# Kernel tuning notes

Measured on AMD Instinct MI355X. Metric: run time of the kernel, lower is better.

Reference implementation:

```python
import jax, jax.numpy as jnp
import numpy as np

B, S = 16, 32768
LEVELS = (5, 20)
TIME_DIM = 8
NUM_FREQS = 6  # frequency xyz encoder: 3*(1+2*6)=39 dims
HID = 128
IN_DIM = 3 * (1 + 2 * NUM_FREQS) + 2 * TIME_DIM  # 55


def setup_inputs() -> dict:
    key = jax.random.key(0)
    ks = jax.random.split(key, 16)
    time = jax.random.uniform(ks[0], (B,), dtype=jnp.float32)
    xyz = jax.random.uniform(ks[1], (B, S, 3), dtype=jnp.float32) * 2.0 - 1.0  # in [-1,1]
    te0 = jax.random.normal(ks[2], (LEVELS[0] + 1, TIME_DIM), dtype=jnp.float32)
    te1 = jax.random.normal(ks[3], (LEVELS[1] + 1, TIME_DIM), dtype=jnp.float32)
    W0 = jax.random.normal(ks[4], (IN_DIM, HID), dtype=jnp.float32) * 0.05
    b0 = jnp.zeros((HID,), dtype=jnp.float32)
    W1 = jax.random.normal(ks[5], (HID, HID), dtype=jnp.float32) * 0.05
    b1 = jnp.zeros((HID,), dtype=jnp.float32)
    W2 = jax.random.normal(ks[6], (HID, HID), dtype=jnp.float32) * 0.05
    b2 = jnp.zeros((HID,), dtype=jnp.float32)
    Wout = jax.random.normal(ks[7], (HID, 1), dtype=jnp.float32) * 0.05
    bout = jnp.zeros((1,), dtype=jnp.float32)
    return {"time": time, "xyz": xyz, "te0": te0, "te1": te1,
            "W0": W0, "b0": b0, "W1": W1, "b1": b1, "W2": W2, "b2": b2,
            "Wout": Wout, "bout": bout}


def _time_encode(t, emb, L):
    # bucketize t into L uniform intervals on [0,1), lerp between bucket endpoints
    tL = t * L
    idx = jnp.clip(jnp.floor(tL).astype(jnp.int32), 0, L - 1)  # (B,)
    w = (idx + 1).astype(t.dtype) - tL                          # weight for lower endpoint
    lerped = w[:, None] * emb[idx] + (1.0 - w)[:, None] * emb[idx + 1]
    # t >= 1: use last embedding directly (torch fallback branch)
    return jnp.where((t >= 1.0)[:, None], emb[L][None, :], lerped)


def _xyz_encode(x):
    # frequency encoding, include_input, freqs 2^0..2^(NUM_FREQS-1)
    freqs = jnp.asarray(2.0 ** np.arange(NUM_FREQS), dtype=x.dtype)  # (F,)
    xp = x[:, None, :] * freqs[None, :, None]                         # (N, F, 3)
    n = x.shape[0]
    return jnp.concatenate([x, jnp.sin(xp).reshape(n, -1), jnp.cos(xp).reshape(n, -1)], axis=-1)


def reference(time, xyz, te0, te1, W0, b0, W1, b1, W2, b2, Wout, bout):
    s = xyz.shape[1]
    t_enc = jnp.concatenate([_time_encode(time, te0, LEVELS[0]),
                             _time_encode(time, te1, LEVELS[1])], axis=-1)  # (B, 16)
    t_enc = jnp.repeat(t_enc, s, axis=0)          # (B*S, 16)  'B d -> (B S) d'
    pts = (xyz.reshape(-1, 3) + 1.0) / 2.0        # (B*S, 3)
    x = jnp.concatenate([t_enc, _xyz_encode(pts)], axis=1)  # (B*S, 55)
    x = jax.nn.relu(x @ W0 + b0)
    x = jax.nn.relu(x @ W1 + b1)
    x = jax.nn.relu(x @ W2 + b2)
    return x @ Wout + bout  # (B*S, 1)
```

## Files before the change

### kernel.cpp

```cpp
#include <hip/hip_runtime.h>

typedef _Float16 f16;
typedef __attribute__((ext_vector_type(2))) __fp16 fp16x2;
typedef __attribute__((ext_vector_type(8))) _Float16 f16x8;
typedef __attribute__((ext_vector_type(4))) float f32x4;
typedef __attribute__((ext_vector_type(4))) unsigned int u32x4;

#define NPTS   (16 * 32768)
#define W0P_OFF 0
#define W1P_OFF (16 * 1024)
#define W2P_OFF (48 * 1024)
#define WOP_OFF (80 * 1024)
#define FRAGS_BYTES (84 * 1024)
#define B0E_OFF FRAGS_BYTES
#define WS_NEEDED (FRAGS_BYTES + 8192)
#define LDS_TOTAL 4096

__global__ void pack_weights(const float* __restrict__ time, const float* __restrict__ te0,
                             const float* __restrict__ te1, const float* __restrict__ W0,
                             const float* __restrict__ b0, const float* __restrict__ W1,
                             const float* __restrict__ W2, const float* __restrict__ Wout,
                             unsigned char* __restrict__ ws) {
  const int bi = blockIdx.x;
  const int l = threadIdx.x;
  const int g = l >> 4, r16 = l & 15;
  if (bi < 84) {
    const float* W; int obase, fi, kt, mt, kmax; bool natural, outcol;
    if (bi < 16)      { W = W0;   fi = bi;      mt = fi >> 1; kt = fi & 1; obase = W0P_OFF; kmax = 39;  natural = true;  outcol = false; }
    else if (bi < 48) { W = W1;   fi = bi - 16; mt = fi >> 2; kt = fi & 3; obase = W1P_OFF; kmax = 128; natural = false; outcol = false; }
    else if (bi < 80) { W = W2;   fi = bi - 48; mt = fi >> 2; kt = fi & 3; obase = W2P_OFF; kmax = 128; natural = false; outcol = false; }
    else              { W = Wout; fi = bi - 80; mt = 0;       kt = fi;     obase = WOP_OFF; kmax = 128; natural = false; outcol = true;  }
    const int m = mt * 16 + r16;
    f16 vals[8] __attribute__((aligned(16)));
#pragma unroll
    for (int j = 0; j < 8; ++j) {
      const int k = natural ? (kt * 32 + g * 8 + j)
                            : (kt * 32 + (j >> 2) * 16 + g * 4 + (j & 3));
      float v = 0.f;
      if (k < kmax) {
        if (outcol)       v = (m == 0) ? Wout[k] : 0.f;
        else if (natural) v = W[(16 + k) * 128 + m];
        else              v = W[k * 128 + m];
      }
      vals[j] = (f16)v;
    }
    *(u32x4*)(ws + obase + (fi * 64 + l) * 16) = *(const u32x4*)vals;
  } else {
    const int idx = (bi - 84) * 64 + l;
    const int b = idx >> 7, m = idx & 127;
    const float t = time[b];
    float acc = b0[m];
#pragma unroll
    for (int d = 0; d < 16; ++d) {
      const float* emb; int L, dd;
      if (d < 8) { emb = te0; L = 5;  dd = d; }
      else       { emb = te1; L = 20; dd = d - 8; }
      const float tL = t * (float)L;
      int i = (int)floorf(tL);
      i = i < 0 ? 0 : (i > L - 1 ? L - 1 : i);
      const float wlo = (float)(i + 1) - tL;
      float v = wlo * emb[i * 8 + dd] + (1.f - wlo) * emb[(i + 1) * 8 + dd];
      if (t >= 1.f) v = emb[L * 8 + dd];
      acc += v * W0[d * 128 + m];
    }
    ((float*)(ws + B0E_OFF))[b * 128 + m] = acc;
  }
}

__device__ __forceinline__ unsigned int pkmax0(unsigned int x) {
  unsigned int r;
  asm("v_pk_max_f16 %0, %1, %2" : "=v"(r) : "v"(x), "v"(0u));
  return r;
}
__device__ __forceinline__ unsigned int pkrtz(float a, float b) {
  union { fp16x2 h; unsigned int u; } c;
  c.h = __builtin_amdgcn_cvt_pkrtz(a, b);
  return c.u;
}
__device__ __forceinline__ float hwsin_rev(float rev) {
  float r; asm("v_sin_f32 %0, %1" : "=v"(r) : "v"(rev)); return r;
}
__device__ __forceinline__ float hwcos_rev(float rev) {
  float r; asm("v_cos_f32 %0, %1" : "=v"(r) : "v"(rev)); return r;
}

template <int KT>
__device__ __forceinline__ void layer_swapped(const unsigned char* __restrict__ wsrc,
                                              const float* __restrict__ bias,
                                              const f16x8 (&Bin)[KT][4], f16x8 (&Bout)[4][4],
                                              int lane) {
  const int g4 = (lane >> 4) * 4;
  f16x8 A0b[3], A1b[3];
  float4 ba, bb;
  f32x4 acc[2][4];
#pragma unroll
  for (int s = 0; s < 2; ++s) {
    const int mtp = s / KT, kt = s % KT;
    A0b[s] = *(const f16x8*)(wsrc + (((2 * mtp)     * KT + kt) * 64 + lane) * 16);
    A1b[s] = *(const f16x8*)(wsrc + (((2 * mtp + 1) * KT + kt) * 64 + lane) * 16);
  }
#pragma unroll
  for (int s = 0; s < 4 * KT; ++s) {
    const int mtp = s / KT, kt = s % KT, cb = s % 3;
    if (kt == 0) {
      ba = *(const float4*)(bias + mtp * 32 + g4);
      bb = *(const float4*)(bias + mtp * 32 + 16 + g4);
#pragma unroll
      for (int nt = 0; nt < 4; ++nt) {
        acc[0][nt] = (f32x4){ba.x, ba.y, ba.z, ba.w};
        acc[1][nt] = (f32x4){bb.x, bb.y, bb.z, bb.w};
      }
    }
    if (s + 2 < 4 * KT) {
      const int mtp2 = (s + 2) / KT, kt2 = (s + 2) % KT, pb = (s + 2) % 3;
      A0b[pb] = *(const f16x8*)(wsrc + (((2 * mtp2)     * KT + kt2) * 64 + lane) * 16);
      A1b[pb] = *(const f16x8*)(wsrc + (((2 * mtp2 + 1) * KT + kt2) * 64 + lane) * 16);
    }
    __builtin_amdgcn_s_setprio(1);
#pragma unroll
    for (int nt = 0; nt < 4; ++nt)
      acc[0][nt] = __builtin_amdgcn_mfma_f32_16x16x32_f16(A0b[cb], Bin[kt][nt], acc[0][nt], 0, 0, 0);
#pragma unroll
    for (int nt = 0; nt < 4; ++nt)
      acc[1][nt] = __builtin_amdgcn_mfma_f32_16x16x32_f16(A1b[cb], Bin[kt][nt], acc[1][nt], 0, 0, 0);
    __builtin_amdgcn_s_setprio(0);
    if (kt == KT - 1) {
#pragma unroll
      for (int nt = 0; nt < 4; ++nt) {
        union { unsigned int w[4]; f16x8 v; } u;
        u.w[0] = pkmax0(pkrtz(acc[0][nt][0], acc[0][nt][1]));
        u.w[1] = pkmax0(pkrtz(acc[0][nt][2], acc[0][nt][3]));
        u.w[2] = pkmax0(pkrtz(acc[1][nt][0], acc[1][nt][1]));
        u.w[3] = pkmax0(pkrtz(acc[1][nt][2], acc[1][nt][3]));
        Bout[mtp][nt] = u.v;
      }
    }
  }
}

__global__ void __launch_bounds__(64, 1)
mlp_main(const float* __restrict__ xyz, const float* __restrict__ b1,
         const float* __restrict__ b2, const float* __restrict__ bout,
         const unsigned char* __restrict__ ws, float* __restrict__ out) {
  extern __shared__ char lds[];
  const int lane = threadIdx.x;
  const int g = lane >> 4, r16 = lane & 15;

  char* scr = lds;
  const float bo = bout[0];

  const int pbase = blockIdx.x * 64;
  const int p = pbase + lane;

  float ff[40];
  const float xs0 = xyz[p * 3], xs1 = xyz[p * 3 + 1], xs2 = xyz[p * 3 + 2];
  const float pcs[3] = {(xs0 + 1.f) * 0.5f, (xs1 + 1.f) * 0.5f, (xs2 + 1.f) * 0.5f};
  const float INV2PI = 0.15915494309189535f;
#pragma unroll
  for (int c = 0; c < 3; ++c) {
    ff[c] = pcs[c];
    const float rev = pcs[c] * INV2PI;
    float s = hwsin_rev(rev), co = hwcos_rev(rev);
#pragma unroll
    for (int f = 0; f < 6; ++f) {
      ff[3 + f * 3 + c] = s;
      ff[21 + f * 3 + c] = co;
      const float s2 = 2.f * s * co, c2 = 1.f - 2.f * s * s;
      s = s2; co = c2;
    }
  }
  ff[39] = 0.f;
  unsigned int fw[32];
#pragma unroll
  for (int i = 0; i < 20; ++i) fw[i] = pkrtz(ff[2 * i], ff[2 * i + 1]);
#pragma unroll
  for (int i = 20; i < 32; ++i) fw[i] = 0u;

  f16x8 B0[2][4];
#pragma unroll
  for (int h = 0; h < 2; ++h) {
    if ((lane >> 5) == h) {
#pragma unroll
      for (int s = 0; s < 8; ++s)
        *(u32x4*)(scr + (lane & 31) * 128 + ((s ^ (lane & 7)) * 16)) = ((const u32x4*)fw)[s];
    }
    asm volatile("s_waitcnt lgkmcnt(0)" ::: "memory");
#pragma unroll
    for (int kt = 0; kt < 2; ++kt)
#pragma unroll
      for (int nn = 0; nn < 2; ++nn) {
        const int row = nn * 16 + r16;
        B0[kt][h * 2 + nn] = *(const f16x8*)(scr + row * 128 + (((4 * kt + g) ^ (row & 7)) * 16));
      }
    asm volatile("s_waitcnt lgkmcnt(0)" ::: "memory");
  }

  const float* b0e = (const float*)(ws + B0E_OFF) + (blockIdx.x >> 9) * 128;
  f16x8 Bx[4][4], By[4][4];
  layer_swapped<2>(ws + W0P_OFF, b0e, B0, Bx, lane);
  layer_swapped<4>(ws + W1P_OFF, b1, Bx, By, lane);
  layer_swapped<4>(ws + W2P_OFF, b2, By, Bx, lane);

  f16x8 Ab[4];
#pragma unroll
  for (int kt = 0; kt < 4; ++kt)
    Ab[kt] = *(const f16x8*)(ws + WOP_OFF + (kt * 64 + lane) * 16);
  const f32x4 bovec = (f32x4){bo, bo, bo, bo};
  f32x4 accO[4];
  __builtin_amdgcn_s_setprio(1);
#pragma unroll
  for (int nt = 0; nt < 4; ++nt)
    accO[nt] = __builtin_amdgcn_mfma_f32_16x16x32_f16(Ab[0], Bx[0][nt], bovec, 0, 0, 0);
#pragma unroll
  for (int kt = 1; kt < 4; ++kt) {
#pragma unroll
    for (int nt = 0; nt < 4; ++nt)
      accO[nt] = __builtin_amdgcn_mfma_f32_16x16x32_f16(Ab[kt], Bx[kt][nt], accO[nt], 0, 0, 0);
  }
  __builtin_amdgcn_s_setprio(0);

  const float a0 = __shfl(accO[0][0], r16, 64);
  const float a1 = __shfl(accO[1][0], r16, 64);
  const float a2 = __shfl(accO[2][0], r16, 64);
  const float a3 = __shfl(accO[3][0], r16, 64);
  const float v = g == 0 ? a0 : g == 1 ? a1 : g == 2 ? a2 : a3;
  out[pbase + lane] = v;
}

extern "C" void kernel_launch(void* const* d_in, const int* in_sizes, int n_in,
                              void* d_out, int out_size, void* d_ws, size_t ws_size,
                              hipStream_t stream) {
  const float* time = (const float*)d_in[0];
  const float* xyz  = (const float*)d_in[1];
  const float* te0  = (const float*)d_in[2];
  const float* te1  = (const float*)d_in[3];
  const float* W0   = (const float*)d_in[4];
  const float* b0   = (const float*)d_in[5];
  const float* W1   = (const float*)d_in[6];
  const float* b1   = (const float*)d_in[7];
  const float* W2   = (const float*)d_in[8];
  const float* b2   = (const float*)d_in[9];
  const float* Wout = (const float*)d_in[10];
  const float* bout = (const float*)d_in[11];
  float* out = (float*)d_out;
  unsigned char* ws = (unsigned char*)d_ws;
  if (ws_size < WS_NEEDED) return;

  pack_weights<<<116, 64, 0, stream>>>(time, te0, te1, W0, b0, W1, W2, Wout, ws);
  mlp_main<<<NPTS / 64, 64, LDS_TOTAL, stream>>>(xyz, b1, b2, bout, ws, out);
}
```

Measured before the change: 46.87 us.

## Process two 64-point tiles per wave to reuse weight fragments across MFMAs

Each single-wave block now handles 128 points as two 64-point tiles. Every loaded weight fragment feeds MFMAs for both tiles, halving weight traffic per point and giving the MFMA pipe more independent work per load. The number of blocks halves, and the time-embedding bias index is adjusted to match. The cost is roughly double the accumulator and activation register footprint, which could cause spills or lower occupancy.

```diff
diff --git a/kernel.cpp b/kernel.cpp
--- a/kernel.cpp
+++ b/kernel.cpp
@@ -85,14 +85,15 @@
 }
 
 template <int KT>
-__device__ __forceinline__ void layer_swapped(const unsigned char* __restrict__ wsrc,
-                                              const float* __restrict__ bias,
-                                              const f16x8 (&Bin)[KT][4], f16x8 (&Bout)[4][4],
-                                              int lane) {
+__device__ __forceinline__ void layer_dual(const unsigned char* __restrict__ wsrc,
+                                           const float* __restrict__ bias,
+                                           const f16x8 (&Bin0)[KT][4], const f16x8 (&Bin1)[KT][4],
+                                           f16x8 (&Bout0)[4][4], f16x8 (&Bout1)[4][4],
+                                           int lane) {
   const int g4 = (lane >> 4) * 4;
   f16x8 A0b[3], A1b[3];
   float4 ba, bb;
-  f32x4 acc[2][4];
+  f32x4 acc0[2][4], acc1[2][4];
 #pragma unroll
   for (int s = 0; s < 2; ++s) {
     const int mtp = s / KT, kt = s % KT;
@@ -107,8 +108,10 @@
       bb = *(const float4*)(bias + mtp * 32 + 16 + g4);
 #pragma unroll
       for (int nt = 0; nt < 4; ++nt) {
-        acc[0][nt] = (f32x4){ba.x, ba.y, ba.z, ba.w};
-        acc[1][nt] = (f32x4){bb.x, bb.y, bb.z, bb.w};
+        acc0[0][nt] = (f32x4){ba.x, ba.y, ba.z, ba.w};
+        acc0[1][nt] = (f32x4){bb.x, bb.y, bb.z, bb.w};
+        acc1[0][nt] = (f32x4){ba.x, ba.y, ba.z, ba.w};
+        acc1[1][nt] = (f32x4){bb.x, bb.y, bb.z, bb.w};
       }
     }
     if (s + 2 < 4 * KT) {
@@ -119,20 +122,31 @@
     __builtin_amdgcn_s_setprio(1);
 #pragma unroll
     for (int nt = 0; nt < 4; ++nt)
-      acc[0][nt] = __builtin_amdgcn_mfma_f32_16x16x32_f16(A0b[cb], Bin[kt][nt], acc[0][nt], 0, 0, 0);
-#pragma unroll
-    for (int nt = 0; nt < 4; ++nt)
-      acc[1][nt] = __builtin_amdgcn_mfma_f32_16x16x32_f16(A1b[cb], Bin[kt][nt], acc[1][nt], 0, 0, 0);
+      acc0[0][nt] = __builtin_amdgcn_mfma_f32_16x16x32_f16(A0b[cb], Bin0[kt][nt], acc0[0][nt], 0, 0, 0);
+#pragma unroll
+    for (int nt = 0; nt < 4; ++nt)
+      acc1[0][nt] = __builtin_amdgcn_mfma_f32_16x16x32_f16(A0b[cb], Bin1[kt][nt], acc1[0][nt], 0, 0, 0);
+#pragma unroll
+    for (int nt = 0; nt < 4; ++nt)
+      acc0[1][nt] = __builtin_amdgcn_mfma_f32_16x16x32_f16(A1b[cb], Bin0[kt][nt], acc0[1][nt], 0, 0, 0);
+#pragma unroll
+    for (int nt = 0; nt < 4; ++nt)
+      acc1[1][nt] = __builtin_amdgcn_mfma_f32_16x16x32_f16(A1b[cb], Bin1[kt][nt], acc1[1][nt], 0, 0, 0);
     __builtin_amdgcn_s_setprio(0);
     if (kt == KT - 1) {
 #pragma unroll
       for (int nt = 0; nt < 4; ++nt) {
-        union { unsigned int w[4]; f16x8 v; } u;
-        u.w[0] = pkmax0(pkrtz(acc[0][nt][0], acc[0][nt][1]));
-        u.w[1] = pkmax0(pkrtz(acc[0][nt][2], acc[0][nt][3]));
-        u.w[2] = pkmax0(pkrtz(acc[1][nt][0], acc[1][nt][1]));
-        u.w[3] = pkmax0(pkrtz(acc[1][nt][2], acc[1][nt][3]));
-        Bout[mtp][nt] = u.v;
+        union { unsigned int w[4]; f16x8 v; } u0, u1;
+        u0.w[0] = pkmax0(pkrtz(acc0[0][nt][0], acc0[0][nt][1]));
+        u0.w[1] = pkmax0(pkrtz(acc0[0][nt][2], acc0[0][nt][3]));
+        u0.w[2] = pkmax0(pkrtz(acc0[1][nt][0], acc0[1][nt][1]));
+        u0.w[3] = pkmax0(pkrtz(acc0[1][nt][2], acc0[1][nt][3]));
+        u1.w[0] = pkmax0(pkrtz(acc1[0][nt][0], acc1[0][nt][1]));
+        u1.w[1] = pkmax0(pkrtz(acc1[0][nt][2], acc1[0][nt][3]));
+        u1.w[2] = pkmax0(pkrtz(acc1[1][nt][0], acc1[1][nt][1]));
+        u1.w[3] = pkmax0(pkrtz(acc1[1][nt][2], acc1[1][nt][3]));
+        Bout0[mtp][nt] = u0.v;
+        Bout1[mtp][nt] = u1.v;
       }
     }
   }
@@ -149,82 +163,97 @@
   char* scr = lds;
   const float bo = bout[0];
 
-  const int pbase = blockIdx.x * 64;
-  const int p = pbase + lane;
-
-  float ff[40];
-  const float xs0 = xyz[p * 3], xs1 = xyz[p * 3 + 1], xs2 = xyz[p * 3 + 2];
-  const float pcs[3] = {(xs0 + 1.f) * 0.5f, (xs1 + 1.f) * 0.5f, (xs2 + 1.f) * 0.5f};
+  const int pbase = blockIdx.x * 128;
+
+  f16x8 B0[2][2][4];
   const float INV2PI = 0.15915494309189535f;
 #pragma unroll
-  for (int c = 0; c < 3; ++c) {
-    ff[c] = pcs[c];
-    const float rev = pcs[c] * INV2PI;
-    float s = hwsin_rev(rev), co = hwcos_rev(rev);
-#pragma unroll
-    for (int f = 0; f < 6; ++f) {
-      ff[3 + f * 3 + c] = s;
-      ff[21 + f * 3 + c] = co;
-      const float s2 = 2.f * s * co, c2 = 1.f - 2.f * s * s;
-      s = s2; co = c2;
-    }
-  }
-  ff[39] = 0.f;
-  unsigned int fw[32];
-#pragma unroll
-  for (int i = 0; i < 20; ++i) fw[i] = pkrtz(ff[2 * i], ff[2 * i + 1]);
-#pragma unroll
-  for (int i = 20; i < 32; ++i) fw[i] = 0u;
-
-  f16x8 B0[2][4];
-#pragma unroll
-  for (int h = 0; h < 2; ++h) {
-    if ((lane >> 5) == h) {
-#pragma unroll
-      for (int s = 0; s < 8; ++s)
-        *(u32x4*)(scr + (lane & 31) * 128 + ((s ^ (lane & 7)) * 16)) = ((const u32x4*)fw)[s];
-    }
-    asm volatile("s_waitcnt lgkmcnt(0)" ::: "memory");
-#pragma unroll
-    for (int kt = 0; kt < 2; ++kt)
-#pragma unroll
-      for (int nn = 0; nn < 2; ++nn) {
-        const int row = nn * 16 + r16;
-        B0[kt][h * 2 + nn] = *(const f16x8*)(scr + row * 128 + (((4 * kt + g) ^ (row & 7)) * 16));
-      }
-    asm volatile("s_waitcnt lgkmcnt(0)" ::: "memory");
-  }
-
-  const float* b0e = (const float*)(ws + B0E_OFF) + (blockIdx.x >> 9) * 128;
-  f16x8 Bx[4][4], By[4][4];
-  layer_swapped<2>(ws + W0P_OFF, b0e, B0, Bx, lane);
-  layer_swapped<4>(ws + W1P_OFF, b1, Bx, By, lane);
-  layer_swapped<4>(ws + W2P_OFF, b2, By, Bx, lane);
+  for (int t = 0; t < 2; ++t) {
+    const int p = pbase + t * 64 + lane;
+    float ff[40];
+    const float xs0 = xyz[p * 3], xs1 = xyz[p * 3 + 1], xs2 = xyz[p * 3 + 2];
+    const float pcs[3] = {(xs0 + 1.f) * 0.5f, (xs1 + 1.f) * 0.5f, (xs2 + 1.f) * 0.5f};
+#pragma unroll
+    for (int c = 0; c < 3; ++c) {
+      ff[c] = pcs[c];
+      const float rev = pcs[c] * INV2PI;
+      float s = hwsin_rev(rev), co = hwcos_rev(rev);
+#pragma unroll
+      for (int f = 0; f < 6; ++f) {
+        ff[3 + f * 3 + c] = s;
+        ff[21 + f * 3 + c] = co;
+        const float s2 = 2.f * s * co, c2 = 1.f - 2.f * s * s;
+        s = s2; co = c2;
+      }
+    }
+    ff[39] = 0.f;
+    unsigned int fw[32];
+#pragma unroll
+    for (int i = 0; i < 20; ++i) fw[i] = pkrtz(ff[2 * i], ff[2 * i + 1]);
+#pragma unroll
+    for (int i = 20; i < 32; ++i) fw[i] = 0u;
+
+#pragma unroll
+    for (int h = 0; h < 2; ++h) {
+      if ((lane >> 5) == h) {
+#pragma unroll
+        for (int s = 0; s < 8; ++s)
+          *(u32x4*)(scr + (lane & 31) * 128 + ((s ^ (lane & 7)) * 16)) = ((const u32x4*)fw)[s];
+      }
+      asm volatile("s_waitcnt lgkmcnt(0)" ::: "memory");
+#pragma unroll
+      for (int kt = 0; kt < 2; ++kt)
+#pragma unroll
+        for (int nn = 0; nn < 2; ++nn) {
+          const int row = nn * 16 + r16;
+          B0[t][kt][h * 2 + nn] = *(const f16x8*)(scr + row * 128 + (((4 * kt + g) ^ (row & 7)) * 16));
+        }
+      asm volatile("s_waitcnt lgkmcnt(0)" ::: "memory");
+    }
+  }
+
+  const float* b0e = (const float*)(ws + B0E_OFF) + (blockIdx.x >> 8) * 128;
+  f16x8 Bx0[4][4], Bx1[4][4], By0[4][4], By1[4][4];
+  layer_dual<2>(ws + W0P_OFF, b0e, B0[0], B0[1], Bx0, Bx1, lane);
+  layer_dual<4>(ws + W1P_OFF, b1, Bx0, Bx1, By0, By1, lane);
+  layer_dual<4>(ws + W2P_OFF, b2, By0, By1, Bx0, Bx1, lane);
 
   f16x8 Ab[4];
 #pragma unroll
   for (int kt = 0; kt < 4; ++kt)
     Ab[kt] = *(const f16x8*)(ws + WOP_OFF + (kt * 64 + lane) * 16);
   const f32x4 bovec = (f32x4){bo, bo, bo, bo};
-  f32x4 accO[4];
+  f32x4 accO0[4], accO1[4];
   __builtin_amdgcn_s_setprio(1);
 #pragma unroll
-  for (int nt = 0; nt < 4; ++nt)
-    accO[nt] = __builtin_amdgcn_mfma_f32_16x16x32_f16(Ab[0], Bx[0][nt], bovec, 0, 0, 0);
+  for (int nt = 0; nt < 4; ++nt) {
+    accO0[nt] = __builtin_amdgcn_mfma_f32_16x16x32_f16(Ab[0], Bx0[0][nt], bovec, 0, 0, 0);
+    accO1[nt] = __builtin_amdgcn_mfma_f32_16x16x32_f16(Ab[0], Bx1[0][nt], bovec, 0, 0, 0);
+  }
 #pragma unroll
   for (int kt = 1; kt < 4; ++kt) {
 #pragma unroll
-    for (int nt = 0; nt < 4; ++nt)
-      accO[nt] = __builtin_amdgcn_mfma_f32_16x16x32_f16(Ab[kt], Bx[kt][nt], accO[nt], 0, 0, 0);
+    for (int nt = 0; nt < 4; ++nt) {
+      accO0[nt] = __builtin_amdgcn_mfma_f32_16x16x32_f16(Ab[kt], Bx0[kt][nt], accO0[nt], 0, 0, 0);
+      accO1[nt] = __builtin_amdgcn_mfma_f32_16x16x32_f16(Ab[kt], Bx1[kt][nt], accO1[nt], 0, 0, 0);
+    }
   }
   __builtin_amdgcn_s_setprio(0);
 
-  const float a0 = __shfl(accO[0][0], r16, 64);
-  const float a1 = __shfl(accO[1][0], r16, 64);
-  const float a2 = __shfl(accO[2][0], r16, 64);
-  const float a3 = __shfl(accO[3][0], r16, 64);
-  const float v = g == 0 ? a0 : g == 1 ? a1 : g == 2 ? a2 : a3;
-  out[pbase + lane] = v;
+  {
+    const float a0 = __shfl(accO0[0][0], r16, 64);
+    const float a1 = __shfl(accO0[1][0], r16, 64);
+    const float a2 = __shfl(accO0[2][0], r16, 64);
+    const float a3 = __shfl(accO0[3][0], r16, 64);
+    out[pbase + lane] = g == 0 ? a0 : g == 1 ? a1 : g == 2 ? a2 : a3;
+  }
+  {
+    const float a0 = __shfl(accO1[0][0], r16, 64);
+    const float a1 = __shfl(accO1[1][0], r16, 64);
+    const float a2 = __shfl(accO1[2][0], r16, 64);
+    const float a3 = __shfl(accO1[3][0], r16, 64);
+    out[pbase + 64 + lane] = g == 0 ? a0 : g == 1 ? a1 : g == 2 ? a2 : a3;
+  }
 }
 
 extern "C" void kernel_launch(void* const* d_in, const int* in_sizes, int n_in,
@@ -247,5 +276,5 @@
   if (ws_size < WS_NEEDED) return;
 
   pack_weights<<<116, 64, 0, stream>>>(time, te0, te1, W0, b0, W1, W2, Wout, ws);
-  mlp_main<<<NPTS / 64, 64, LDS_TOTAL, stream>>>(xyz, b1, b2, bout, ws, out);
-}
+  mlp_main<<<NPTS / 128, 64, LDS_TOTAL, stream>>>(xyz, b1, b2, bout, ws, out);
+}
```

Result: slower. 51.45 us (+9.8%).
